# Kernel tuning notes

Hardware: AMD Instinct MI355X
Metric: run time of the kernel (lower is better)

Reference implementation:

```python
import jax, jax.numpy as jnp
import numpy as np

CROSS_PRUNE = 0.1  # matches init_kwargs cross_prune

N, T, D, M = 100000, 64, 128, 8


def setup_inputs() -> dict:
    key = jax.random.key(0)
    k1, k2, k3, k4 = jax.random.split(key, 4)
    x = jax.random.normal(k1, (N, D), dtype=jnp.float32)          # graph node features
    mats = jax.random.normal(k2, (M, T, D), dtype=jnp.float32) * 0.1  # cross mats (kaiming-ish scale)
    head_w = jax.random.normal(k3, (M,), dtype=jnp.float32) * 0.3     # task_head.weight [1, M] squeezed
    head_b = jax.random.normal(k4, (), dtype=jnp.float32) * 0.1       # task_head.bias
    return {"x": x, "mats": mats, "head_w": head_w, "head_b": head_b}


def reference(x, mats, head_w, head_b):
    # Original: for each mat m, cross_dot_m = mat_m @ x.T  -> M mats of [T, N];
    # then per-(i,j): task_head([cross_dot_m[i,j] for m]) = sum_m w_m * cross_dot_m[i,j] + b.
    # Linearity lets us contract the head weight into the mats first (identical math,
    # avoids materializing the [M, T, N] stack the torch code builds element-by-element).
    w_mat = jnp.einsum('m,mtd->td', head_w, mats)          # [T, D]
    cross_dot = jnp.einsum('td,nd->tn', w_mat, x) + head_b  # [T, N]
    cross_sim = jax.nn.sigmoid(cross_dot)
    # prune: entries below threshold -> 0 (dense adjacency; edge_index extraction in the
    # original is just nonzero() over this matrix, which has data-dependent shape)
    cross_adj = jnp.where(cross_sim < CROSS_PRUNE, jnp.zeros_like(cross_sim), cross_sim)
    return cross_adj
```

## Files before the change

kernel.cpp:

```cpp
#include <hip/hip_runtime.h>

#define N_NODES 100000
#define T_DIM 64
#define D_DIM 128
#define M_MATS 8
#define CROSS_PRUNE 0.1f

typedef __attribute__((ext_vector_type(8))) short bf16x8;
typedef __attribute__((ext_vector_type(4))) float f32x4;

__device__ __forceinline__ unsigned short f2bf(float f) {
    unsigned int u = __float_as_uint(f);
    u += 0x7FFFu + ((u >> 16) & 1u);
    return (unsigned short)(u >> 16);
}
__device__ __forceinline__ float bf2f(unsigned short h) {
    return __uint_as_float(((unsigned int)h) << 16);
}

__global__ __launch_bounds__(256) void wmat_kernel(const float* __restrict__ mats,
                                                   const float* __restrict__ head_w,
                                                   float* __restrict__ w) {
    int i = blockIdx.x * 256 + threadIdx.x;
    if (i < T_DIM * D_DIM) {
        float acc = 0.f;
#pragma unroll
        for (int m = 0; m < M_MATS; ++m)
            acc += head_w[m] * mats[m * (T_DIM * D_DIM) + i];
        w[i] = acc;
    }
}

#define HSTR 72
__global__ __launch_bounds__(256, 4) void cross_kernel(const float* __restrict__ x,
                                                       const float* __restrict__ w,
                                                       const float* __restrict__ head_b_p,
                                                       float* __restrict__ out) {
    __shared__ unsigned short xh[64 * HSTR];
    __shared__ unsigned short xm[64 * HSTR];
    __shared__ unsigned short xl[64 * HSTR];

    const int tid = threadIdx.x;
    const int n0 = blockIdx.x * 64;

    const int srow = tid >> 2;
    const int scol = (tid & 3) * 16;
    const int gn_s = n0 + srow;
    const float* xrow = x + (size_t)gn_s * D_DIM + scol;

    float4 p0[4], p1[4];
#pragma unroll
    for (int j = 0; j < 4; ++j) {
        p0[j] = make_float4(0.f, 0.f, 0.f, 0.f);
        p1[j] = p0[j];
        if (gn_s < N_NODES) {
            p0[j] = *reinterpret_cast<const float4*>(xrow + j * 4);
            p1[j] = *reinterpret_cast<const float4*>(xrow + 64 + j * 4);
        }
    }

#define SPLIT_STORE(P, EO)                                                     \
    {                                                                          \
        float fv[4] = {(P).x, (P).y, (P).z, (P).w};                            \
        ushort4 H, M, L;                                                       \
        unsigned short* Hp = &H.x; unsigned short* Mp = &M.x;                  \
        unsigned short* Lp = &L.x;                                             \
        _Pragma("unroll")                                                      \
        for (int e = 0; e < 4; ++e) {                                          \
            unsigned short h_ = f2bf(fv[e]); float r1_ = fv[e] - bf2f(h_);     \
            unsigned short m_ = f2bf(r1_);   float r2_ = r1_ - bf2f(m_);      \
            Hp[e] = h_; Mp[e] = m_; Lp[e] = f2bf(r2_);                         \
        }                                                                      \
        *reinterpret_cast<ushort4*>(&xh[EO]) = H;                              \
        *reinterpret_cast<ushort4*>(&xm[EO]) = M;                              \
        *reinterpret_cast<ushort4*>(&xl[EO]) = L;                              \
    }

#pragma unroll
    for (int j = 0; j < 4; ++j)
        SPLIT_STORE(p0[j], srow * HSTR + scol + j * 4);
    __syncthreads();

    const int lane = tid & 63;
    const int tg = tid >> 6;
    const int r = lane & 15;
    const int q = lane >> 4;

    f32x4 acc[4];
#pragma unroll
    for (int nt = 0; nt < 4; ++nt) acc[nt] = (f32x4){0.f, 0.f, 0.f, 0.f};

#pragma unroll
    for (int half = 0; half < 2; ++half) {
        if (half == 1) {
            __syncthreads();
#pragma unroll
            for (int j = 0; j < 4; ++j)
                SPLIT_STORE(p1[j], srow * HSTR + scol + j * 4);
            __syncthreads();
        }

        bf16x8 ah[2], am[2], al[2];
#pragma unroll
        for (int k4 = 0; k4 < 2; ++k4) {
            const float* wp = w + (tg * 16 + r) * D_DIM + half * 64 + k4 * 32 + q * 8;
            float4 wa = *reinterpret_cast<const float4*>(wp);
            float4 wb = *reinterpret_cast<const float4*>(wp + 4);
            float wf[8] = {wa.x, wa.y, wa.z, wa.w, wb.x, wb.y, wb.z, wb.w};
#pragma unroll
            for (int j = 0; j < 8; ++j) {
                unsigned short h_ = f2bf(wf[j]); float r1_ = wf[j] - bf2f(h_);
                unsigned short m_ = f2bf(r1_);   float r2_ = r1_ - bf2f(m_);
                ah[k4][j] = (short)h_; am[k4][j] = (short)m_; al[k4][j] = (short)f2bf(r2_);
            }
        }

#pragma unroll
        for (int k4 = 0; k4 < 2; ++k4) {
#pragma unroll
            for (int nt = 0; nt < 4; ++nt) {
                int eo = (nt * 16 + r) * HSTR + k4 * 32 + q * 8;
                bf16x8 bh = *reinterpret_cast<const bf16x8*>(&xh[eo]);
                bf16x8 bm = *reinterpret_cast<const bf16x8*>(&xm[eo]);
                bf16x8 bl = *reinterpret_cast<const bf16x8*>(&xl[eo]);
                acc[nt] = __builtin_amdgcn_mfma_f32_16x16x32_bf16(ah[k4], bh, acc[nt], 0, 0, 0);
                acc[nt] = __builtin_amdgcn_mfma_f32_16x16x32_bf16(ah[k4], bm, acc[nt], 0, 0, 0);
                acc[nt] = __builtin_amdgcn_mfma_f32_16x16x32_bf16(am[k4], bh, acc[nt], 0, 0, 0);
                acc[nt] = __builtin_amdgcn_mfma_f32_16x16x32_bf16(ah[k4], bl, acc[nt], 0, 0, 0);
                acc[nt] = __builtin_amdgcn_mfma_f32_16x16x32_bf16(al[k4], bh, acc[nt], 0, 0, 0);
                acc[nt] = __builtin_amdgcn_mfma_f32_16x16x32_bf16(am[k4], bm, acc[nt], 0, 0, 0);
            }
        }
    }

    const float hb = head_b_p[0];
#pragma unroll
    for (int nt = 0; nt < 4; ++nt) {
        int n = n0 + nt * 16 + r;
        if (n < N_NODES) {
#pragma unroll
            for (int i = 0; i < 4; ++i) {
                int t = tg * 16 + q * 4 + i;
                float v = acc[nt][i] + hb;
                float s = 1.0f / (1.0f + __expf(-v));
                if (s < CROSS_PRUNE) s = 0.0f;
                out[(size_t)t * N_NODES + n] = s;
            }
        }
    }
#undef SPLIT_STORE
}

extern "C" void kernel_launch(void* const* d_in, const int* in_sizes, int n_in,
                              void* d_out, int out_size, void* d_ws, size_t ws_size,
                              hipStream_t stream) {
    const float* x      = (const float*)d_in[0];
    const float* mats   = (const float*)d_in[1];
    const float* head_w = (const float*)d_in[2];
    const float* head_b = (const float*)d_in[3];
    float* out = (float*)d_out;
    float* w   = (float*)d_ws;

    hipLaunchKernelGGL(wmat_kernel, dim3((T_DIM * D_DIM + 255) / 256), dim3(256), 0, stream,
                       mats, head_w, w);

    int nblk = (N_NODES + 63) / 64;
    hipLaunchKernelGGL(cross_kernel, dim3(nblk), dim3(256), 0, stream,
                       x, w, head_b, out);
}
```

Measured before the change: 35.59 us.

## Swizzle LDS layout, use 16-byte split stores, hip bf16 conversions, raise occupancy

Replaces the padded shared-memory layout (stride 72) with an unpadded 64-wide layout using an XOR swizzle on 16-byte units, so LDS drops to 24KB per block and stores become 16-byte vectors. The float-to-bf16 splitting now uses the hip_bfloat16 intrinsics, which may map to hardware conversion instructions. Launch bounds are raised to 5 blocks per CU to allow more occupancy. Risks include register pressure from the tighter bound and the swizzle not fully removing bank conflicts.

```diff
diff --git a/kernel.cpp b/kernel.cpp
--- a/kernel.cpp
+++ b/kernel.cpp
@@ -1,4 +1,5 @@
 #include <hip/hip_runtime.h>
+#include <hip/hip_bf16.h>
 
 #define N_NODES 100000
 #define T_DIM 64
@@ -8,14 +9,20 @@
 
 typedef __attribute__((ext_vector_type(8))) short bf16x8;
 typedef __attribute__((ext_vector_type(4))) float f32x4;
+typedef __attribute__((ext_vector_type(8))) unsigned short ushort8;
 
-__device__ __forceinline__ unsigned short f2bf(float f) {
-    unsigned int u = __float_as_uint(f);
-    u += 0x7FFFu + ((u >> 16) & 1u);
-    return (unsigned short)(u >> 16);
-}
-__device__ __forceinline__ float bf2f(unsigned short h) {
-    return __uint_as_float(((unsigned int)h) << 16);
+__device__ __forceinline__ void split3(float v, unsigned short& h,
+                                       unsigned short& m, unsigned short& l) {
+    __hip_bfloat16 bh = __float2bfloat16(v);
+    float fh = __bfloat162float(bh);
+    float r1 = v - fh;
+    __hip_bfloat16 bm = __float2bfloat16(r1);
+    float fm = __bfloat162float(bm);
+    float r2 = r1 - fm;
+    __hip_bfloat16 bl = __float2bfloat16(r2);
+    h = __builtin_bit_cast(unsigned short, bh);
+    m = __builtin_bit_cast(unsigned short, bm);
+    l = __builtin_bit_cast(unsigned short, bl);
 }
 
 __global__ __launch_bounds__(256) void wmat_kernel(const float* __restrict__ mats,
@@ -31,14 +38,13 @@
     }
 }
 
-#define HSTR 72
-__global__ __launch_bounds__(256, 4) void cross_kernel(const float* __restrict__ x,
+__global__ __launch_bounds__(256, 5) void cross_kernel(const float* __restrict__ x,
                                                        const float* __restrict__ w,
                                                        const float* __restrict__ head_b_p,
                                                        float* __restrict__ out) {
-    __shared__ unsigned short xh[64 * HSTR];
-    __shared__ unsigned short xm[64 * HSTR];
-    __shared__ unsigned short xl[64 * HSTR];
+    __shared__ unsigned short xh[64 * 64];
+    __shared__ unsigned short xm[64 * 64];
+    __shared__ unsigned short xl[64 * 64];
 
     const int tid = threadIdx.x;
     const int n0 = blockIdx.x * 64;
@@ -59,26 +65,32 @@
         }
     }
 
-#define SPLIT_STORE(P, EO)                                                     \
-    {                                                                          \
-        float fv[4] = {(P).x, (P).y, (P).z, (P).w};                            \
-        ushort4 H, M, L;                                                       \
-        unsigned short* Hp = &H.x; unsigned short* Mp = &M.x;                  \
-        unsigned short* Lp = &L.x;                                             \
-        _Pragma("unroll")                                                      \
-        for (int e = 0; e < 4; ++e) {                                          \
-            unsigned short h_ = f2bf(fv[e]); float r1_ = fv[e] - bf2f(h_);     \
-            unsigned short m_ = f2bf(r1_);   float r2_ = r1_ - bf2f(m_);      \
-            Hp[e] = h_; Mp[e] = m_; Lp[e] = f2bf(r2_);                         \
-        }                                                                      \
-        *reinterpret_cast<ushort4*>(&xh[EO]) = H;                              \
-        *reinterpret_cast<ushort4*>(&xm[EO]) = M;                              \
-        *reinterpret_cast<ushort4*>(&xl[EO]) = L;                              \
+#define SPLIT_STORE16(P)                                                        \
+    {                                                                           \
+        float fv[16];                                                           \
+        _Pragma("unroll")                                                       \
+        for (int j = 0; j < 4; ++j) {                                           \
+            fv[j * 4 + 0] = (P)[j].x; fv[j * 4 + 1] = (P)[j].y;                 \
+            fv[j * 4 + 2] = (P)[j].z; fv[j * 4 + 3] = (P)[j].w;                 \
+        }                                                                       \
+        _Pragma("unroll")                                                       \
+        for (int u = 0; u < 2; ++u) {                                           \
+            ushort8 H, M, L;                                                    \
+            _Pragma("unroll")                                                   \
+            for (int e = 0; e < 8; ++e) {                                       \
+                unsigned short h_, m_, l_;                                      \
+                split3(fv[u * 8 + e], h_, m_, l_);                              \
+                H[e] = h_; M[e] = m_; L[e] = l_;                                \
+            }                                                                   \
+            int unit = srow * 8 + (tid & 3) * 2 + u;                            \
+            int byte = (unit << 4) ^ ((srow & 7) << 4);                         \
+            *reinterpret_cast<ushort8*>(reinterpret_cast<char*>(xh) + byte) = H;\
+            *reinterpret_cast<ushort8*>(reinterpret_cast<char*>(xm) + byte) = M;\
+            *reinterpret_cast<ushort8*>(reinterpret_cast<char*>(xl) + byte) = L;\
+        }                                                                       \
     }
 
-#pragma unroll
-    for (int j = 0; j < 4; ++j)
-        SPLIT_STORE(p0[j], srow * HSTR + scol + j * 4);
+    SPLIT_STORE16(p0);
     __syncthreads();
 
     const int lane = tid & 63;
@@ -94,9 +106,7 @@
     for (int half = 0; half < 2; ++half) {
         if (half == 1) {
             __syncthreads();
-#pragma unroll
-            for (int j = 0; j < 4; ++j)
-                SPLIT_STORE(p1[j], srow * HSTR + scol + j * 4);
+            SPLIT_STORE16(p1);
             __syncthreads();
         }
 
@@ -109,9 +119,9 @@
             float wf[8] = {wa.x, wa.y, wa.z, wa.w, wb.x, wb.y, wb.z, wb.w};
 #pragma unroll
             for (int j = 0; j < 8; ++j) {
-                unsigned short h_ = f2bf(wf[j]); float r1_ = wf[j] - bf2f(h_);
-                unsigned short m_ = f2bf(r1_);   float r2_ = r1_ - bf2f(m_);
-                ah[k4][j] = (short)h_; am[k4][j] = (short)m_; al[k4][j] = (short)f2bf(r2_);
+                unsigned short h_, m_, l_;
+                split3(wf[j], h_, m_, l_);
+                ah[k4][j] = (short)h_; am[k4][j] = (short)m_; al[k4][j] = (short)l_;
             }
         }
 
@@ -119,10 +129,13 @@
         for (int k4 = 0; k4 < 2; ++k4) {
 #pragma unroll
             for (int nt = 0; nt < 4; ++nt) {
-                int eo = (nt * 16 + r) * HSTR + k4 * 32 + q * 8;
-                bf16x8 bh = *reinterpret_cast<const bf16x8*>(&xh[eo]);
-                bf16x8 bm = *reinterpret_cast<const bf16x8*>(&xm[eo]);
-                bf16x8 bl = *reinterpret_cast<const bf16x8*>(&xl[eo]);
+                int byte = (((nt * 16 + r) * 64 + k4 * 32 + q * 8) << 1) ^ ((r & 7) << 4);
+                bf16x8 bh = *reinterpret_cast<const bf16x8*>(
+                    reinterpret_cast<const char*>(xh) + byte);
+                bf16x8 bm = *reinterpret_cast<const bf16x8*>(
+                    reinterpret_cast<const char*>(xm) + byte);
+                bf16x8 bl = *reinterpret_cast<const bf16x8*>(
+                    reinterpret_cast<const char*>(xl) + byte);
                 acc[nt] = __builtin_amdgcn_mfma_f32_16x16x32_bf16(ah[k4], bh, acc[nt], 0, 0, 0);
                 acc[nt] = __builtin_amdgcn_mfma_f32_16x16x32_bf16(ah[k4], bm, acc[nt], 0, 0, 0);
                 acc[nt] = __builtin_amdgcn_mfma_f32_16x16x32_bf16(am[k4], bh, acc[nt], 0, 0, 0);
@@ -148,7 +161,7 @@
             }
         }
     }
-#undef SPLIT_STORE
+#undef SPLIT_STORE16
 }
 
 extern "C" void kernel_launch(void* const* d_in, const int* in_sizes, int n_in,
```

Result: faster. 31.99 us (-10.1%).
